# Performance work log

Hardware: AMD Instinct MI355X
Metric: run time of the kernel (lower is better)

## Reference

```python
import jax, jax.numpy as jnp
import numpy as np

BLOCK = 8  # block_shape = (8, 8)
INT8_MAX = 127.0  # torch.iinfo(int8).max used by pyblaz bin()


def _dct_matrix(n: int) -> jnp.ndarray:
    """Orthonormal DCT-II matrix D[element, frequency] (pyblaz cosine transform)."""
    e = jnp.arange(n, dtype=jnp.float32)[:, None]
    f = jnp.arange(n, dtype=jnp.float32)[None, :]
    scale = jnp.where(f == 0, jnp.sqrt(1.0 / n), jnp.sqrt(2.0 / n))
    return scale * jnp.cos(jnp.pi * (2.0 * e + 1.0) * f / (2.0 * n))


def setup_inputs() -> dict:
    key = jax.random.key(0)
    x = jax.random.normal(key, (4096, 4096), dtype=jnp.float32)
    return {"x": x}


def reference(x):
    H, W = x.shape
    nb0, nb1 = H // BLOCK, W // BLOCK
    # block splitting: (H, W) -> (nb0, nb1, 8, 8)
    blocked = x.reshape(nb0, BLOCK, nb1, BLOCK).transpose(0, 2, 1, 3)
    D = _dct_matrix(BLOCK)
    # blockwise separable orthogonal transform (same math as the 4D transformer
    # tensor einsum in PyBlaz.blockwise_transform, which is D ⊗ D)
    coeffs = jnp.einsum("abef,eg,fh->abgh", blocked, D, D)
    # mask is all-ones (mask=None) -> masked select == flatten block dims
    flat = coeffs.reshape(nb0, nb1, BLOCK * BLOCK)
    # bin(): per-block max magnitude, then quantize to int8 indices
    biggest = jnp.max(jnp.abs(flat), axis=-1)  # (nb0, nb1)
    safe = jnp.where(biggest == 0, 1.0, biggest)
    indices = jnp.round(flat / safe[..., None] * INT8_MAX).astype(jnp.int8)
    return biggest, indices
```

## Files before the change

kernel.cpp:

```cpp
#include <hip/hip_runtime.h>


#define IMG_W 4096
#define NB    512
#define NBLK  (NB * NB)
#define WG    64

typedef float f32x4 __attribute__((ext_vector_type(4)));

__global__ __launch_bounds__(WG) void dct_quant_kernel(
    const float* __restrict__ x,
    float* __restrict__ out_big,
    float* __restrict__ out_idx)
{
    __shared__ __align__(16) float T[8 * 72];
    __shared__ float Dl[64];
    __shared__ unsigned int Sg[8 * 18];

    const int l = threadIdx.x;
    const int b = l & 7;
    const int g = l >> 3;

    {
        float rev = (float)((2 * g + 1) * b) * (1.0f / 32.0f);
        rev = rev - floorf(rev);
        float c;
        asm("v_cos_f32 %0, %1" : "=v"(c) : "v"(rev));
        const float sc = (b == 0) ? 0.35355339059327373f : 0.5f;
        Dl[g * 8 + b] = sc * c;
    }

    const int gblk0 = blockIdx.x * 8;
    const int gblk  = gblk0 + b;
    const int bi = gblk >> 9;
    const int bj = gblk & (NB - 1);

    const float s0 = 0.35355339059327373f;
    const float d1 = 0.49039264020161522f;
    const float d2 = 0.46193976625564337f;
    const float d3 = 0.41573480615127262f;
    const float d4 = 0.35355339059327379f;
    const float d5 = 0.27778511650980114f;
    const float d6 = 0.19134171618254492f;
    const float d7 = 0.09754516100806413f;
    const float D[8][8] = {
        { s0,  d1,  d2,  d3,  d4,  d5,  d6,  d7},
        { s0,  d3,  d6, -d7, -d4, -d1, -d2, -d5},
        { s0,  d5, -d6, -d1, -d4,  d7,  d2,  d3},
        { s0,  d7, -d2, -d5,  d4,  d3, -d6, -d1},
        { s0, -d7, -d2,  d5,  d4, -d3, -d6,  d1},
        { s0, -d5, -d6,  d1, -d4, -d7,  d2, -d3},
        { s0, -d3,  d6,  d7, -d4,  d1, -d2,  d5},
        { s0, -d1,  d2, -d3,  d4, -d5,  d6, -d7},
    };

    const float* p = x + (size_t)(bi * 8 + g) * IMG_W + (size_t)bj * 8;
    const float4 r0 = *reinterpret_cast<const float4*>(p);
    const float4 r1 = *reinterpret_cast<const float4*>(p + 4);
    const float row[8] = {r0.x, r0.y, r0.z, r0.w, r1.x, r1.y, r1.z, r1.w};

    float* tw = &T[b * 72 + g * 8];
#pragma unroll
    for (int h = 0; h < 8; ++h) {
        float acc = row[0] * D[0][h];
#pragma unroll
        for (int f = 1; f < 8; ++f) acc = fmaf(row[f], D[f][h], acc);
        tw[h ^ g] = acc;
    }

    __syncthreads();

    float Dg[8];
#pragma unroll
    for (int e = 0; e < 8; ++e) Dg[e] = Dl[e * 8 + g];

    float C[8];
#pragma unroll
    for (int h = 0; h < 8; ++h) C[h] = 0.0f;

    const float* tr = &T[b * 72];
#pragma unroll
    for (int e = 0; e < 8; ++e) {
        const float4 a0 = *reinterpret_cast<const float4*>(tr + e * 8);
        const float4 a1 = *reinterpret_cast<const float4*>(tr + e * 8 + 4);
        const float rj[8] = {a0.x, a0.y, a0.z, a0.w, a1.x, a1.y, a1.z, a1.w};
#pragma unroll
        for (int h = 0; h < 8; ++h)
            C[h] = fmaf(Dg[e], rj[h ^ e], C[h]);
    }

    float m = fabsf(C[0]);
#pragma unroll
    for (int h = 1; h < 8; ++h) m = fmaxf(m, fabsf(C[h]));
    m = fmaxf(m, __shfl_xor(m, 8, 64));
    m = fmaxf(m, __shfl_xor(m, 16, 64));
    m = fmaxf(m, __shfl_xor(m, 32, 64));

    if (g == 0)
        __builtin_nontemporal_store(m, &out_big[gblk0 + b]);

    const float safe = (m == 0.0f) ? 1.0f : m;
    const float inv  = 127.0f / safe;

    int q[8];
#pragma unroll
    for (int h = 0; h < 8; ++h) q[h] = (int)rintf(C[h] * inv);
    const unsigned int w0 = (q[0] & 0xff) | ((q[1] & 0xff) << 8) |
                            ((q[2] & 0xff) << 16) | ((unsigned)(q[3] & 0xff) << 24);
    const unsigned int w1 = (q[4] & 0xff) | ((q[5] & 0xff) << 8) |
                            ((q[6] & 0xff) << 16) | ((unsigned)(q[7] & 0xff) << 24);
    Sg[b * 18 + g * 2]     = w0;
    Sg[b * 18 + g * 2 + 1] = w1;

    __syncthreads();

    f32x4* og = reinterpret_cast<f32x4*>(out_idx + (size_t)gblk0 * 64);
#pragma unroll
    for (int kk = 0; kk < 2; ++kk) {
        const int k = kk * 64 + l;
        const unsigned int w = Sg[(k >> 4) * 18 + (k & 15)];
        f32x4 qv;
        qv.x = (float)(int)(signed char)(w        & 0xff);
        qv.y = (float)(int)(signed char)((w >> 8)  & 0xff);
        qv.z = (float)(int)(signed char)((w >> 16) & 0xff);
        qv.w = (float)(int)(signed char)(w >> 24);
        __builtin_nontemporal_store(qv, &og[k]);
    }
}

extern "C" void kernel_launch(void* const* d_in, const int* in_sizes, int n_in,
                              void* d_out, int out_size, void* d_ws, size_t ws_size,
                              hipStream_t stream) {
    const float* x = (const float*)d_in[0];
    float* out = (float*)d_out;
    float* out_big = out;
    float* out_idx = out + NBLK;

    dct_quant_kernel<<<NBLK / 8, WG, 0, stream>>>(x, out_big, out_idx);
}
```

Before: 25.29 us.

## Process eight block-groups per workgroup with register prefetch of next rows

Each workgroup now loops over 8 consecutive groups of 8 DCT blocks instead of handling one group, so the grid shrinks 8x. The next iteration's input rows are loaded into registers before the current group is computed. This spreads the per-workgroup setup cost (DCT matrix in LDS) over more work and overlaps global loads with compute. In exchange it adds extra barriers per iteration, uses more registers, and gives fewer workgroups to hide latency with.

```diff
diff --git a/kernel.cpp b/kernel.cpp
--- a/kernel.cpp
+++ b/kernel.cpp
@@ -5,10 +5,11 @@
 #define NB    512
 #define NBLK  (NB * NB)
 #define WG    64
+#define ITERS 8
 
 typedef float f32x4 __attribute__((ext_vector_type(4)));
 
-__global__ __launch_bounds__(WG) void dct_quant_kernel(
+__global__ __launch_bounds__(WG, 4) void dct_quant_kernel(
     const float* __restrict__ x,
     float* __restrict__ out_big,
     float* __restrict__ out_idx)
@@ -29,11 +30,11 @@
         const float sc = (b == 0) ? 0.35355339059327373f : 0.5f;
         Dl[g * 8 + b] = sc * c;
     }
+    __syncthreads();
 
-    const int gblk0 = blockIdx.x * 8;
-    const int gblk  = gblk0 + b;
-    const int bi = gblk >> 9;
-    const int bj = gblk & (NB - 1);
+    float Dg[8];
+#pragma unroll
+    for (int e = 0; e < 8; ++e) Dg[e] = Dl[e * 8 + g];
 
     const float s0 = 0.35355339059327373f;
     const float d1 = 0.49039264020161522f;
@@ -54,77 +55,92 @@
         { s0, -d1,  d2, -d3,  d4, -d5,  d6, -d7},
     };
 
-    const float* p = x + (size_t)(bi * 8 + g) * IMG_W + (size_t)bj * 8;
-    const float4 r0 = *reinterpret_cast<const float4*>(p);
-    const float4 r1 = *reinterpret_cast<const float4*>(p + 4);
-    const float row[8] = {r0.x, r0.y, r0.z, r0.w, r1.x, r1.y, r1.z, r1.w};
+    const int wgid = blockIdx.x;
+    const int bi   = wgid >> 3;
+    const float* rowbase = x + (size_t)(bi * 8 + g) * IMG_W
+                             + (size_t)(wgid & 7) * 512 + (size_t)b * 8;
 
-    float* tw = &T[b * 72 + g * 8];
+    float4 a0 = *reinterpret_cast<const float4*>(rowbase);
+    float4 a1 = *reinterpret_cast<const float4*>(rowbase + 4);
+
 #pragma unroll
-    for (int h = 0; h < 8; ++h) {
-        float acc = row[0] * D[0][h];
+    for (int it = 0; it < ITERS; ++it) {
+        float4 n0 = a0, n1 = a1;
+        if (it + 1 < ITERS) {
+            n0 = *reinterpret_cast<const float4*>(rowbase + (it + 1) * 64);
+            n1 = *reinterpret_cast<const float4*>(rowbase + (it + 1) * 64 + 4);
+        }
+
+        const int gblk0 = wgid * 64 + it * 8;
+
+        const float row[8] = {a0.x, a0.y, a0.z, a0.w, a1.x, a1.y, a1.z, a1.w};
+        float* tw = &T[b * 72 + g * 8];
 #pragma unroll
-        for (int f = 1; f < 8; ++f) acc = fmaf(row[f], D[f][h], acc);
-        tw[h ^ g] = acc;
-    }
+        for (int h = 0; h < 8; ++h) {
+            float acc = row[0] * D[0][h];
+#pragma unroll
+            for (int f = 1; f < 8; ++f) acc = fmaf(row[f], D[f][h], acc);
+            tw[h ^ g] = acc;
+        }
 
-    __syncthreads();
+        __syncthreads();
 
-    float Dg[8];
+        float C[8];
 #pragma unroll
-    for (int e = 0; e < 8; ++e) Dg[e] = Dl[e * 8 + g];
+        for (int h = 0; h < 8; ++h) C[h] = 0.0f;
 
-    float C[8];
+        const float* tr = &T[b * 72];
 #pragma unroll
-    for (int h = 0; h < 8; ++h) C[h] = 0.0f;
+        for (int e = 0; e < 8; ++e) {
+            const float4 c0 = *reinterpret_cast<const float4*>(tr + e * 8);
+            const float4 c1 = *reinterpret_cast<const float4*>(tr + e * 8 + 4);
+            const float rj[8] = {c0.x, c0.y, c0.z, c0.w, c1.x, c1.y, c1.z, c1.w};
+#pragma unroll
+            for (int h = 0; h < 8; ++h)
+                C[h] = fmaf(Dg[e], rj[h ^ e], C[h]);
+        }
 
-    const float* tr = &T[b * 72];
+        float m = fabsf(C[0]);
 #pragma unroll
-    for (int e = 0; e < 8; ++e) {
-        const float4 a0 = *reinterpret_cast<const float4*>(tr + e * 8);
-        const float4 a1 = *reinterpret_cast<const float4*>(tr + e * 8 + 4);
-        const float rj[8] = {a0.x, a0.y, a0.z, a0.w, a1.x, a1.y, a1.z, a1.w};
+        for (int h = 1; h < 8; ++h) m = fmaxf(m, fabsf(C[h]));
+        m = fmaxf(m, __shfl_xor(m, 8, 64));
+        m = fmaxf(m, __shfl_xor(m, 16, 64));
+        m = fmaxf(m, __shfl_xor(m, 32, 64));
+
+        if (g == 0)
+            __builtin_nontemporal_store(m, &out_big[gblk0 + b]);
+
+        const float safe = (m == 0.0f) ? 1.0f : m;
+        const float inv  = 127.0f / safe;
+
+        int q[8];
 #pragma unroll
-        for (int h = 0; h < 8; ++h)
-            C[h] = fmaf(Dg[e], rj[h ^ e], C[h]);
-    }
+        for (int h = 0; h < 8; ++h) q[h] = (int)rintf(C[h] * inv);
+        const unsigned int w0 = (q[0] & 0xff) | ((q[1] & 0xff) << 8) |
+                                ((q[2] & 0xff) << 16) | ((unsigned)(q[3] & 0xff) << 24);
+        const unsigned int w1 = (q[4] & 0xff) | ((q[5] & 0xff) << 8) |
+                                ((q[6] & 0xff) << 16) | ((unsigned)(q[7] & 0xff) << 24);
+        Sg[b * 18 + g * 2]     = w0;
+        Sg[b * 18 + g * 2 + 1] = w1;
 
-    float m = fabsf(C[0]);
+        __syncthreads();
+
+        f32x4* og = reinterpret_cast<f32x4*>(out_idx + (size_t)gblk0 * 64);
 #pragma unroll
-    for (int h = 1; h < 8; ++h) m = fmaxf(m, fabsf(C[h]));
-    m = fmaxf(m, __shfl_xor(m, 8, 64));
-    m = fmaxf(m, __shfl_xor(m, 16, 64));
-    m = fmaxf(m, __shfl_xor(m, 32, 64));
+        for (int kk = 0; kk < 2; ++kk) {
+            const int k = kk * 64 + l;
+            const unsigned int w = Sg[(k >> 4) * 18 + (k & 15)];
+            f32x4 qv;
+            qv.x = (float)(int)(signed char)(w        & 0xff);
+            qv.y = (float)(int)(signed char)((w >> 8)  & 0xff);
+            qv.z = (float)(int)(signed char)((w >> 16) & 0xff);
+            qv.w = (float)(int)(signed char)(w >> 24);
+            __builtin_nontemporal_store(qv, &og[k]);
+        }
 
-    if (g == 0)
-        __builtin_nontemporal_store(m, &out_big[gblk0 + b]);
+        __syncthreads();
 
-    const float safe = (m == 0.0f) ? 1.0f : m;
-    const float inv  = 127.0f / safe;
-
-    int q[8];
-#pragma unroll
-    for (int h = 0; h < 8; ++h) q[h] = (int)rintf(C[h] * inv);
-    const unsigned int w0 = (q[0] & 0xff) | ((q[1] & 0xff) << 8) |
-                            ((q[2] & 0xff) << 16) | ((unsigned)(q[3] & 0xff) << 24);
-    const unsigned int w1 = (q[4] & 0xff) | ((q[5] & 0xff) << 8) |
-                            ((q[6] & 0xff) << 16) | ((unsigned)(q[7] & 0xff) << 24);
-    Sg[b * 18 + g * 2]     = w0;
-    Sg[b * 18 + g * 2 + 1] = w1;
-
-    __syncthreads();
-
-    f32x4* og = reinterpret_cast<f32x4*>(out_idx + (size_t)gblk0 * 64);
-#pragma unroll
-    for (int kk = 0; kk < 2; ++kk) {
-        const int k = kk * 64 + l;
-        const unsigned int w = Sg[(k >> 4) * 18 + (k & 15)];
-        f32x4 qv;
-        qv.x = (float)(int)(signed char)(w        & 0xff);
-        qv.y = (float)(int)(signed char)((w >> 8)  & 0xff);
-        qv.z = (float)(int)(signed char)((w >> 16) & 0xff);
-        qv.w = (float)(int)(signed char)(w >> 24);
-        __builtin_nontemporal_store(qv, &og[k]);
+        a0 = n0; a1 = n1;
     }
 }
 
@@ -136,5 +152,5 @@
     float* out_big = out;
     float* out_idx = out + NBLK;
 
-    dct_quant_kernel<<<NBLK / 8, WG, 0, stream>>>(x, out_big, out_idx);
+    dct_quant_kernel<<<NBLK / 64, WG, 0, stream>>>(x, out_big, out_idx);
 }
```

New measurement: 27.30 us. 1.08x slower.
